# Kernel optimization log

Measured on AMD Instinct MI355X. Metric: run time of the kernel, lower is better.

Reference implementation:

```python
import jax, jax.numpy as jnp
import numpy as np

B, CIN, COUT, WDIM, H, W = 16, 512, 3, 512, 128, 128
FC_GAIN = float(1.0 / np.sqrt(WDIM))        # FullyConnectedLayer weight gain (lr_mult=1)
WEIGHT_GAIN = float(1.0 / np.sqrt(CIN * 1))  # 1 / sqrt(in_channels * kernel_size**2)
CLAMP = 256.0


def setup_inputs() -> dict:
    key = jax.random.key(0)
    k = jax.random.split(key, 5)
    return {
        "x": jax.random.normal(k[0], (B, CIN, H, W), jnp.float32),
        "w": jax.random.normal(k[1], (B, WDIM), jnp.float32),
        # StyleSplit: FullyConnectedLayer(w_dim, 3*in_channels, bias_init=1)
        "affine_W": jax.random.normal(k[2], (3 * CIN, WDIM), jnp.float32),
        "affine_b": jnp.ones((3 * CIN,), jnp.float32),
        # 1x1 conv weight, init 0.1*randn, stored as [COUT, CIN]
        "conv_w": 0.1 * jax.random.normal(k[3], (COUT, CIN), jnp.float32),
        "conv_b": jnp.zeros((COUT,), jnp.float32),
    }


def reference(x, w, affine_W, affine_b, conv_w, conv_b):
    # StyleSplit affine: FC (with 1/sqrt(in) weight gain) -> m1*m2 + m3
    s = w @ affine_W.T * FC_GAIN + affine_b            # [B, 3*CIN]
    m1, m2, m3 = jnp.split(s, 3, axis=1)               # each [B, CIN]
    styles = (m1 * m2 + m3) * WEIGHT_GAIN              # [B, CIN]
    # Modulated 1x1 conv, demodulate=False: per-sample weight = conv_w * styles
    out = jnp.einsum('bchw,oc,bc->bohw', x, conv_w, styles)  # [B, COUT, H, W]
    # bias_act: linear activation + bias + clamp
    out = out + conv_b[None, :, None, None]
    return jnp.clip(out, -CLAMP, CLAMP)
```

## Files before the change

### kernel.cpp

```cpp
#include <hip/hip_runtime.h>
#include <hip/hip_bf16.h>

#define B_      16
#define CIN_    512
#define COUT_   3
#define WDIM_   512
#define HW_     16384
#define FC_GAIN     0.044194173824159216f
#define WEIGHT_GAIN 0.044194173824159216f
#define CLAMP_  256.0f

__global__ __launch_bounds__(64) void style_kernel(
    const float* __restrict__ w,
    const float* __restrict__ affine_W,
    const float* __restrict__ affine_b,
    const float* __restrict__ conv_w,
    float4* __restrict__ eff4) {
  const int bc   = blockIdx.x;
  const int b    = bc >> 9;
  const int c    = bc & 511;
  const int lane = threadIdx.x;

  const float* wb = w + b * WDIM_;
  const float* r1 = affine_W + (size_t)c * WDIM_;
  const float* r2 = affine_W + (size_t)(c + CIN_) * WDIM_;
  const float* r3 = affine_W + (size_t)(c + 2 * CIN_) * WDIM_;

  float p1 = 0.f, p2 = 0.f, p3 = 0.f;
#pragma unroll
  for (int j = 0; j < WDIM_ / 64; ++j) {
    const int k = j * 64 + lane;
    const float wk = wb[k];
    p1 = fmaf(wk, r1[k], p1);
    p2 = fmaf(wk, r2[k], p2);
    p3 = fmaf(wk, r3[k], p3);
  }
#pragma unroll
  for (int off = 32; off > 0; off >>= 1) {
    p1 += __shfl_down(p1, off);
    p2 += __shfl_down(p2, off);
    p3 += __shfl_down(p3, off);
  }
  if (lane == 0) {
    const float s1 = p1 * FC_GAIN + affine_b[c];
    const float s2 = p2 * FC_GAIN + affine_b[c + CIN_];
    const float s3 = p3 * FC_GAIN + affine_b[c + 2 * CIN_];
    const float style = (s1 * s2 + s3) * WEIGHT_GAIN;
    float4 e;
    e.x = conv_w[0 * CIN_ + c] * style;
    e.y = conv_w[1 * CIN_ + c] * style;
    e.z = conv_w[2 * CIN_ + c] * style;
    e.w = 0.f;
    eff4[bc] = e;
  }
}

__global__ __launch_bounds__(256) void conv_kernel(
    const float* __restrict__ x,
    const float4* __restrict__ eff4,
    const float* __restrict__ conv_b,
    float* __restrict__ out) {
  __shared__ float4 s_eff[CIN_];

  const int b    = blockIdx.x >> 4;
  const int tile = blockIdx.x & 15;
  const int tid  = threadIdx.x;

  s_eff[tid]       = eff4[b * CIN_ + tid];
  s_eff[tid + 256] = eff4[b * CIN_ + tid + 256];
  __syncthreads();

  const float4* xb = (const float4*)x + ((size_t)b * CIN_) * (HW_ / 4)
                     + (size_t)tile * 256 + tid;

  float a0x = 0.f, a0y = 0.f, a0z = 0.f, a0w = 0.f;
  float a1x = 0.f, a1y = 0.f, a1z = 0.f, a1w = 0.f;
  float a2x = 0.f, a2y = 0.f, a2z = 0.f, a2w = 0.f;

#pragma unroll 8
  for (int c = 0; c < CIN_; ++c) {
    const float4 xv = xb[(size_t)c * (HW_ / 4)];
    const float4 e  = s_eff[c];
    a0x = fmaf(xv.x, e.x, a0x); a0y = fmaf(xv.y, e.x, a0y);
    a0z = fmaf(xv.z, e.x, a0z); a0w = fmaf(xv.w, e.x, a0w);
    a1x = fmaf(xv.x, e.y, a1x); a1y = fmaf(xv.y, e.y, a1y);
    a1z = fmaf(xv.z, e.y, a1z); a1w = fmaf(xv.w, e.y, a1w);
    a2x = fmaf(xv.x, e.z, a2x); a2y = fmaf(xv.y, e.z, a2y);
    a2z = fmaf(xv.z, e.z, a2z); a2w = fmaf(xv.w, e.z, a2w);
  }

  const float b0 = conv_b[0], b1 = conv_b[1], b2 = conv_b[2];
#define CLMP(v, bb) fminf(fmaxf((v) + (bb), -CLAMP_), CLAMP_)
  float4 o0 = make_float4(CLMP(a0x, b0), CLMP(a0y, b0), CLMP(a0z, b0), CLMP(a0w, b0));
  float4 o1 = make_float4(CLMP(a1x, b1), CLMP(a1y, b1), CLMP(a1z, b1), CLMP(a1w, b1));
  float4 o2 = make_float4(CLMP(a2x, b2), CLMP(a2y, b2), CLMP(a2z, b2), CLMP(a2w, b2));
#undef CLMP

  float4* op = (float4*)out + ((size_t)b * COUT_) * (HW_ / 4)
               + (size_t)tile * 256 + tid;
  op[0]                = o0;
  op[1 * (HW_ / 4)]    = o1;
  op[2 * (HW_ / 4)]    = o2;
}

extern "C" void kernel_launch(void* const* d_in, const int* in_sizes, int n_in,
                              void* d_out, int out_size, void* d_ws, size_t ws_size,
                              hipStream_t stream) {
  const float* x        = (const float*)d_in[0];
  const float* w        = (const float*)d_in[1];
  const float* affine_W = (const float*)d_in[2];
  const float* affine_b = (const float*)d_in[3];
  const float* conv_w   = (const float*)d_in[4];
  const float* conv_b   = (const float*)d_in[5];
  float* out = (float*)d_out;

  float4* eff4 = (float4*)d_ws;

  style_kernel<<<B_ * CIN_, 64, 0, stream>>>(w, affine_W, affine_b, conv_w, eff4);
  conv_kernel<<<B_ * 16, 256, 0, stream>>>(x, eff4, conv_b, out);
}
```

Before: 669.2 us.

## Split channel reduction across waves to quadruple conv kernel grid

```diff
diff --git a/kernel.cpp b/kernel.cpp
--- a/kernel.cpp
+++ b/kernel.cpp
@@ -1,11 +1,10 @@
 #include <hip/hip_runtime.h>
-#include <hip/hip_bf16.h>
 
 #define B_      16
 #define CIN_    512
 #define COUT_   3
 #define WDIM_   512
-#define HW_     16384
+#define HW4_    4096
 #define FC_GAIN     0.044194173824159216f
 #define WEIGHT_GAIN 0.044194173824159216f
 #define CLAMP_  256.0f
@@ -61,26 +60,31 @@
     const float* __restrict__ conv_b,
     float* __restrict__ out) {
   __shared__ float4 s_eff[CIN_];
+  __shared__ float4 s_red[4][64][COUT_];
 
-  const int b    = blockIdx.x >> 4;
-  const int tile = blockIdx.x & 15;
+  const int b    = blockIdx.x >> 6;
+  const int tile = blockIdx.x & 63;
   const int tid  = threadIdx.x;
+  const int wave = tid >> 6;
+  const int lane = tid & 63;
 
   s_eff[tid]       = eff4[b * CIN_ + tid];
   s_eff[tid + 256] = eff4[b * CIN_ + tid + 256];
   __syncthreads();
 
-  const float4* xb = (const float4*)x + ((size_t)b * CIN_) * (HW_ / 4)
-                     + (size_t)tile * 256 + tid;
+  const float4* xb = (const float4*)x
+      + ((size_t)b * CIN_ + (size_t)wave * 128) * HW4_
+      + (size_t)tile * 64 + lane;
+  const float4* ep = &s_eff[wave * 128];
 
   float a0x = 0.f, a0y = 0.f, a0z = 0.f, a0w = 0.f;
   float a1x = 0.f, a1y = 0.f, a1z = 0.f, a1w = 0.f;
   float a2x = 0.f, a2y = 0.f, a2z = 0.f, a2w = 0.f;
 
 #pragma unroll 8
-  for (int c = 0; c < CIN_; ++c) {
-    const float4 xv = xb[(size_t)c * (HW_ / 4)];
-    const float4 e  = s_eff[c];
+  for (int c = 0; c < CIN_ / 4; ++c) {
+    const float4 xv = xb[(size_t)c * HW4_];
+    const float4 e  = ep[c];
     a0x = fmaf(xv.x, e.x, a0x); a0y = fmaf(xv.y, e.x, a0y);
     a0z = fmaf(xv.z, e.x, a0z); a0w = fmaf(xv.w, e.x, a0w);
     a1x = fmaf(xv.x, e.y, a1x); a1y = fmaf(xv.y, e.y, a1y);
@@ -89,18 +93,29 @@
     a2z = fmaf(xv.z, e.z, a2z); a2w = fmaf(xv.w, e.z, a2w);
   }
 
-  const float b0 = conv_b[0], b1 = conv_b[1], b2 = conv_b[2];
-#define CLMP(v, bb) fminf(fmaxf((v) + (bb), -CLAMP_), CLAMP_)
-  float4 o0 = make_float4(CLMP(a0x, b0), CLMP(a0y, b0), CLMP(a0z, b0), CLMP(a0w, b0));
-  float4 o1 = make_float4(CLMP(a1x, b1), CLMP(a1y, b1), CLMP(a1z, b1), CLMP(a1w, b1));
-  float4 o2 = make_float4(CLMP(a2x, b2), CLMP(a2y, b2), CLMP(a2z, b2), CLMP(a2w, b2));
+  s_red[wave][lane][0] = make_float4(a0x, a0y, a0z, a0w);
+  s_red[wave][lane][1] = make_float4(a1x, a1y, a1z, a1w);
+  s_red[wave][lane][2] = make_float4(a2x, a2y, a2z, a2w);
+  __syncthreads();
+
+  if (tid < 64 * COUT_) {
+    const int o = tid >> 6;
+    const int l = tid & 63;
+    const float4 r0 = s_red[0][l][o];
+    const float4 r1 = s_red[1][l][o];
+    const float4 r2 = s_red[2][l][o];
+    const float4 r3 = s_red[3][l][o];
+    const float bb = conv_b[o];
+#define CLMP(v) fminf(fmaxf((v) + bb, -CLAMP_), CLAMP_)
+    float4 res = make_float4(CLMP(r0.x + r1.x + r2.x + r3.x),
+                             CLMP(r0.y + r1.y + r2.y + r3.y),
+                             CLMP(r0.z + r1.z + r2.z + r3.z),
+                             CLMP(r0.w + r1.w + r2.w + r3.w));
 #undef CLMP
-
-  float4* op = (float4*)out + ((size_t)b * COUT_) * (HW_ / 4)
-               + (size_t)tile * 256 + tid;
-  op[0]                = o0;
-  op[1 * (HW_ / 4)]    = o1;
-  op[2 * (HW_ / 4)]    = o2;
+    float4* op = (float4*)out + ((size_t)b * COUT_ + o) * HW4_
+                 + (size_t)tile * 64 + l;
+    *op = res;
+  }
 }
 
 extern "C" void kernel_launch(void* const* d_in, const int* in_sizes, int n_in,
@@ -117,5 +132,5 @@
   float4* eff4 = (float4*)d_ws;
 
   style_kernel<<<B_ * CIN_, 64, 0, stream>>>(w, affine_W, affine_b, conv_w, eff4);
-  conv_kernel<<<B_ * 16, 256, 0, stream>>>(x, eff4, conv_b, out);
+  conv_kernel<<<B_ * 64, 256, 0, stream>>>(x, eff4, conv_b, out);
 }
```

Result: no change. 677.7 us (+1.3%).

## Split channel reduction across blocks with partial sums and separate reduce kernel

Applied to the files above, without the earlier changes.

```diff
diff --git a/kernel.cpp b/kernel.cpp
--- a/kernel.cpp
+++ b/kernel.cpp
@@ -1,14 +1,20 @@
 #include <hip/hip_runtime.h>
-#include <hip/hip_bf16.h>
 
 #define B_      16
 #define CIN_    512
 #define COUT_   3
 #define WDIM_   512
-#define HW_     16384
+#define HW4_    4096
 #define FC_GAIN     0.044194173824159216f
 #define WEIGHT_GAIN 0.044194173824159216f
 #define CLAMP_  256.0f
+
+#define NGRP_   16
+#define CPG_    32
+#define NTILE_  4
+#define TSZ_    1024
+#define K_      4
+#define PART_OFF_ 131072
 
 __global__ __launch_bounds__(64) void style_kernel(
     const float* __restrict__ w,
@@ -55,52 +61,95 @@
   }
 }
 
-__global__ __launch_bounds__(256) void conv_kernel(
+#define FMA4(acc, xv, s)                                      \
+  acc.x = fmaf(xv.x, (s), acc.x); acc.y = fmaf(xv.y, (s), acc.y); \
+  acc.z = fmaf(xv.z, (s), acc.z); acc.w = fmaf(xv.w, (s), acc.w);
+
+__global__ __launch_bounds__(256, 4) void conv_partial_kernel(
     const float* __restrict__ x,
     const float4* __restrict__ eff4,
-    const float* __restrict__ conv_b,
-    float* __restrict__ out) {
-  __shared__ float4 s_eff[CIN_];
+    float4* __restrict__ part) {
+  __shared__ float4 s_eff[CPG_];
 
-  const int b    = blockIdx.x >> 4;
-  const int tile = blockIdx.x & 15;
+  const int bx   = blockIdx.x;
+  const int b    = bx >> 6;
+  const int tile = (bx >> 4) & 3;
+  const int g    = bx & 15;
   const int tid  = threadIdx.x;
 
-  s_eff[tid]       = eff4[b * CIN_ + tid];
-  s_eff[tid + 256] = eff4[b * CIN_ + tid + 256];
+  if (tid < CPG_) s_eff[tid] = eff4[b * CIN_ + g * CPG_ + tid];
   __syncthreads();
 
-  const float4* xb = (const float4*)x + ((size_t)b * CIN_) * (HW_ / 4)
-                     + (size_t)tile * 256 + tid;
+  const float4* xb = (const float4*)x
+      + ((size_t)b * CIN_ + (size_t)g * CPG_) * HW4_
+      + (size_t)tile * TSZ_ + tid;
 
-  float a0x = 0.f, a0y = 0.f, a0z = 0.f, a0w = 0.f;
-  float a1x = 0.f, a1y = 0.f, a1z = 0.f, a1w = 0.f;
-  float a2x = 0.f, a2y = 0.f, a2z = 0.f, a2w = 0.f;
-
-#pragma unroll 8
-  for (int c = 0; c < CIN_; ++c) {
-    const float4 xv = xb[(size_t)c * (HW_ / 4)];
-    const float4 e  = s_eff[c];
-    a0x = fmaf(xv.x, e.x, a0x); a0y = fmaf(xv.y, e.x, a0y);
-    a0z = fmaf(xv.z, e.x, a0z); a0w = fmaf(xv.w, e.x, a0w);
-    a1x = fmaf(xv.x, e.y, a1x); a1y = fmaf(xv.y, e.y, a1y);
-    a1z = fmaf(xv.z, e.y, a1z); a1w = fmaf(xv.w, e.y, a1w);
-    a2x = fmaf(xv.x, e.z, a2x); a2y = fmaf(xv.y, e.z, a2y);
-    a2z = fmaf(xv.z, e.z, a2z); a2w = fmaf(xv.w, e.z, a2w);
+  float4 a0[K_], a1[K_], a2[K_];
+#pragma unroll
+  for (int k = 0; k < K_; ++k) {
+    a0[k] = make_float4(0.f, 0.f, 0.f, 0.f);
+    a1[k] = make_float4(0.f, 0.f, 0.f, 0.f);
+    a2[k] = make_float4(0.f, 0.f, 0.f, 0.f);
   }
 
-  const float b0 = conv_b[0], b1 = conv_b[1], b2 = conv_b[2];
-#define CLMP(v, bb) fminf(fmaxf((v) + (bb), -CLAMP_), CLAMP_)
-  float4 o0 = make_float4(CLMP(a0x, b0), CLMP(a0y, b0), CLMP(a0z, b0), CLMP(a0w, b0));
-  float4 o1 = make_float4(CLMP(a1x, b1), CLMP(a1y, b1), CLMP(a1z, b1), CLMP(a1w, b1));
-  float4 o2 = make_float4(CLMP(a2x, b2), CLMP(a2y, b2), CLMP(a2z, b2), CLMP(a2w, b2));
+#pragma unroll 2
+  for (int c = 0; c < CPG_; ++c) {
+    float4 xv[K_];
+#pragma unroll
+    for (int k = 0; k < K_; ++k) xv[k] = xb[(size_t)c * HW4_ + k * 256];
+    const float4 e = s_eff[c];
+#pragma unroll
+    for (int k = 0; k < K_; ++k) {
+      FMA4(a0[k], xv[k], e.x);
+      FMA4(a1[k], xv[k], e.y);
+      FMA4(a2[k], xv[k], e.z);
+    }
+  }
+
+  float4* pb = part + ((size_t)(b * NGRP_ + g) * COUT_) * HW4_
+               + (size_t)tile * TSZ_ + tid;
+#pragma unroll
+  for (int k = 0; k < K_; ++k) {
+    pb[k * 256]                = a0[k];
+    pb[k * 256 + 1 * HW4_]     = a1[k];
+    pb[k * 256 + 2 * HW4_]     = a2[k];
+  }
+}
+
+__global__ __launch_bounds__(256) void reduce_kernel(
+    const float4* __restrict__ part,
+    const float* __restrict__ conv_b,
+    float4* __restrict__ out4) {
+  const int bx   = blockIdx.x;
+  const int b    = bx / 12;
+  const int r    = bx % 12;
+  const int o    = r >> 2;
+  const int tile = r & 3;
+  const int tid  = threadIdx.x;
+
+  float4 acc[K_];
+#pragma unroll
+  for (int k = 0; k < K_; ++k) acc[k] = make_float4(0.f, 0.f, 0.f, 0.f);
+
+  for (int g = 0; g < NGRP_; ++g) {
+    const float4* pp = part + ((size_t)(b * NGRP_ + g) * COUT_ + o) * HW4_
+                       + (size_t)tile * TSZ_ + tid;
+#pragma unroll
+    for (int k = 0; k < K_; ++k) {
+      const float4 v = pp[k * 256];
+      acc[k].x += v.x; acc[k].y += v.y; acc[k].z += v.z; acc[k].w += v.w;
+    }
+  }
+
+  const float bb = conv_b[o];
+#define CLMP(v) fminf(fmaxf((v) + bb, -CLAMP_), CLAMP_)
+  float4* op = out4 + ((size_t)b * COUT_ + o) * HW4_ + (size_t)tile * TSZ_ + tid;
+#pragma unroll
+  for (int k = 0; k < K_; ++k) {
+    op[k * 256] = make_float4(CLMP(acc[k].x), CLMP(acc[k].y),
+                              CLMP(acc[k].z), CLMP(acc[k].w));
+  }
 #undef CLMP
-
-  float4* op = (float4*)out + ((size_t)b * COUT_) * (HW_ / 4)
-               + (size_t)tile * 256 + tid;
-  op[0]                = o0;
-  op[1 * (HW_ / 4)]    = o1;
-  op[2 * (HW_ / 4)]    = o2;
 }
 
 extern "C" void kernel_launch(void* const* d_in, const int* in_sizes, int n_in,
@@ -115,7 +164,9 @@
   float* out = (float*)d_out;
 
   float4* eff4 = (float4*)d_ws;
+  float4* part = (float4*)d_ws + PART_OFF_;
 
   style_kernel<<<B_ * CIN_, 64, 0, stream>>>(w, affine_W, affine_b, conv_w, eff4);
-  conv_kernel<<<B_ * 16, 256, 0, stream>>>(x, eff4, conv_b, out);
+  conv_partial_kernel<<<B_ * NTILE_ * NGRP_, 256, 0, stream>>>(x, eff4, part);
+  reduce_kernel<<<B_ * COUT_ * NTILE_, 256, 0, stream>>>(part, conv_b, (float4*)out);
 }
```

Measured after the change: 699.0 us. 1.04x slower.
